# Kernel tuning notes

Hardware: AMD Instinct MI355X
Metric: run time of the kernel (lower is better)

Reference implementation:

```python
import jax, jax.numpy as jnp
import numpy as np

B, T, E, H, V = 64, 128, 256, 1024, 8000

def setup_inputs() -> dict:
    key = jax.random.key(0)
    ks = jax.random.split(key, 18)
    s = 0.1
    f = lambda k, shp: (jax.random.normal(k, shp) * s).astype(jnp.float32)
    return {
        "x": jax.random.randint(ks[0], (B, T), 0, V),
        "given_num": 64,
        "emb": f(ks[1], (V, E)),
        "Wi": f(ks[2], (E, H)), "Ui": f(ks[3], (H, H)), "bi": f(ks[4], (H,)),
        "Wf": f(ks[5], (E, H)), "Uf": f(ks[6], (H, H)), "bf": f(ks[7], (H,)),
        "Wog": f(ks[8], (E, H)), "Uog": f(ks[9], (H, H)), "bog": f(ks[10], (H,)),
        "Wc": f(ks[11], (E, H)), "Uc": f(ks[12], (H, H)), "bc": f(ks[13], (H,)),
        "Wo": f(ks[14], (H, V)), "bo": f(ks[15], (V,)),
    }

def reference(x, given_num, emb, Wi, Ui, bi, Wf, Uf, bf, Wog, Uog, bog, Wc, Uc, bc, Wo, bo):
    # NOTE: the torch source overwrites processed_x[i] AFTER it has been consumed,
    # so the recurrence is fully teacher-forced on x; sampling only fills gen_x
    # for steps >= given_num. We reproduce exactly that.
    px = jnp.transpose(emb[x], (1, 0, 2))               # [T,B,E] teacher embeddings
    Wcat = jnp.concatenate([Wi, Wf, Wog, Wc], axis=1)    # [E,4H] fused input-gate weights
    Ucat = jnp.concatenate([Ui, Uf, Uog, Uc], axis=1)    # [H,4H] fused hidden-gate weights
    bcat = jnp.concatenate([bi, bf, bog, bc])            # [4H]
    xw = jnp.einsum('tbe,eh->tbh', px, Wcat) + bcat      # [T,B,4H] one big GEMM upfront
    keys = jax.random.split(jax.random.key(1), T)        # per-step sampling keys

    def step(carry, inp):
        h, c = carry
        xw_t, i, xtok, k = inp
        z = xw_t + h @ Ucat                              # [B,4H] fused gate pre-activations
        i_g, f_g, o_g, c_hat = jnp.split(z, 4, axis=-1)
        c = jax.nn.sigmoid(f_g) * c + jax.nn.sigmoid(i_g) * jnp.tanh(c_hat)
        h = jax.nn.sigmoid(o_g) * jnp.tanh(c)
        logits = h @ Wo + bo                             # [B,V]
        samp = jax.random.categorical(k, logits)         # = multinomial over softmax
        tok = jnp.where(i < given_num, xtok, samp)
        return (h, c), tok

    h0 = jnp.zeros((B, H), jnp.float32)
    c0 = jnp.zeros((B, H), jnp.float32)
    _, toks = jax.lax.scan(step, (h0, c0), (xw, jnp.arange(T), x.T, keys))
    return toks.T                                        # [B,T] int tokens (gen_x)
```

## Files before the change

kernel.cpp:

```cpp
#include <hip/hip_runtime.h>
#include <hip/hip_cooperative_groups.h>
#include <cstdint>
#include <cstddef>

#define TT 128
#define BB 64
#define EE 256
#define HH 1024
#define VV 8000
#define LSTRIDE 132

__device__ __forceinline__ uint32_t rotl32(uint32_t v, int r){ return (v<<r)|(v>>(32-r)); }

__device__ __forceinline__ void tf2x32(uint32_t k0, uint32_t k1, uint32_t x0, uint32_t x1,
                                       uint32_t& y0, uint32_t& y1)
{
  const uint32_t k2 = k0 ^ k1 ^ 0x1BD11BDAu;
  x0 += k0; x1 += k1;
#define TFR(r) { x0 += x1; x1 = rotl32(x1,(r)); x1 ^= x0; }
  TFR(13) TFR(15) TFR(26) TFR(6)   x0 += k1; x1 += k2 + 1u;
  TFR(17) TFR(29) TFR(16) TFR(24)  x0 += k2; x1 += k0 + 2u;
  TFR(13) TFR(15) TFR(26) TFR(6)   x0 += k0; x1 += k1 + 3u;
  TFR(17) TFR(29) TFR(16) TFR(24)  x0 += k1; x1 += k2 + 4u;
  TFR(13) TFR(15) TFR(26) TFR(6)   x0 += k2; x1 += k0 + 5u;
#undef TFR
  y0 = x0; y1 = x1;
}

__device__ __forceinline__ float u01f(uint32_t bits){
  float f = __uint_as_float((bits >> 9) | 0x3f800000u) - 1.0f;
  return (f == 0.0f) ? 1.17549435e-38f : f;
}

__device__ __forceinline__ float xla_tanh(float x){
  float xc = fminf(fmaxf(x, -7.90531110763549805f), 7.90531110763549805f);
  float x2 = __fmul_rn(xc, xc);
  float num = -2.76076847742355e-16f;
  num = __fadd_rn(__fmul_rn(x2, num),  2.00018790482477e-13f);
  num = __fadd_rn(__fmul_rn(x2, num), -8.60467152213735e-11f);
  num = __fadd_rn(__fmul_rn(x2, num),  5.12229709037114e-08f);
  num = __fadd_rn(__fmul_rn(x2, num),  1.48572235717979e-05f);
  num = __fadd_rn(__fmul_rn(x2, num),  6.37261928875436e-04f);
  num = __fadd_rn(__fmul_rn(x2, num),  4.89352455891786e-03f);
  num = __fmul_rn(xc, num);
  float den = 1.19825839466702e-06f;
  den = __fadd_rn(__fmul_rn(x2, den), 1.18534705686654e-04f);
  den = __fadd_rn(__fmul_rn(x2, den), 2.26843463243900e-03f);
  den = __fadd_rn(__fmul_rn(x2, den), 4.89352518554385e-03f);
  float r = __fdiv_rn(num, den);
  return (fabsf(x) < 0.0004f) ? x : r;
}

__device__ __forceinline__ float xla_sigmoid(float x){
  float t = xla_tanh(__fmul_rn(0.5f, x));
  return __fadd_rn(0.5f, __fmul_rn(0.5f, t));
}

__device__ __forceinline__ unsigned long long pack32(float s, int v){
  uint32_t u = __float_as_uint(s);
  u = (u >> 31) ? ~u : (u | 0x80000000u);
  return ((unsigned long long)u << 32) | (unsigned)(8191 - v);
}

#define LGKM0 asm volatile("s_waitcnt lgkmcnt(0)" ::: "memory")

__global__ void initz(float* hfull, unsigned long long* best, int* flags){
  int i = blockIdx.x*256 + threadIdx.x;
  if (i < HH*BB)  hfull[i] = 0.f;
  if (i < TT*BB)  best[i] = 0ull;
  if (i < 256)    flags[i] = 0;
}

__global__ __launch_bounds__(256) void pxgen(
    const int* __restrict__ x, const float* __restrict__ emb, float* __restrict__ px)
{
  int flat = blockIdx.x*256 + threadIdx.x;
  int b = flat & 63;
  int e = (flat >> 6) & 255;
  int t = flat >> 14;
  if (t >= TT) return;
  int tok = x[b*TT + t];
  px[((size_t)t*EE + e)*BB + b] = emb[(size_t)tok*EE + e];
}

__global__ __launch_bounds__(256) void transpose4f(
    const float* __restrict__ g0, const float* __restrict__ g1,
    const float* __restrict__ g2, const float* __restrict__ g3,
    float* __restrict__ out, int R, int C)
{
  const float* in = (blockIdx.y==0)?g0:(blockIdx.y==1)?g1:(blockIdx.y==2)?g2:g3;
  int tilesC = C >> 6;
  int tr = blockIdx.x / tilesC, tc = blockIdx.x % tilesC;
  __shared__ float tile[64][65];
  int tid = threadIdx.x;
  #pragma unroll
  for (int s = 0; s < 16; ++s) {
    int li = s*256 + tid;
    int r = li >> 6, c = li & 63;
    tile[r][c] = in[(size_t)(tr*64 + r)*C + tc*64 + c];
  }
  __syncthreads();
  #pragma unroll
  for (int s = 0; s < 16; ++s) {
    int li = s*256 + tid;
    int c = li >> 6, r = li & 63;
    out[((size_t)blockIdx.y*C + tc*64 + c)*R + tr*64 + r] = tile[r][c];
  }
}

__global__ __launch_bounds__(512) void lstm_rec(
    const float* __restrict__ Wt, const float* __restrict__ Ut,
    const float* __restrict__ bi, const float* __restrict__ bf,
    const float* __restrict__ bog, const float* __restrict__ bc,
    const float* __restrict__ px, float* __restrict__ hfull,
    int* __restrict__ flags)
{
  __shared__ float sA[64*LSTRIDE];
  __shared__ float sB[64*LSTRIDE];
  __shared__ float spx[64*LSTRIDE];
  __shared__ float xch[2304];

  const int tid  = threadIdx.x;
  const int w    = tid >> 6;
  const int lane = tid & 63;
  const int p    = w & 3;
  const int kh   = w >> 2;
  const int ju   = __builtin_amdgcn_readfirstlane(blockIdx.x*4 + p);
  const int sw4  = ((lane >> 3) & 7) << 2;

  const float* Ug0 = Ut + ((size_t)0*HH + ju)*HH;
  const float* Ug1 = Ut + ((size_t)1*HH + ju)*HH;
  const float* Ug2 = Ut + ((size_t)2*HH + ju)*HH;
  const float* Ug3 = Ut + ((size_t)3*HH + ju)*HH;
  const int g0 = 2*kh, g1 = 2*kh + 1;
  const float* W0 = Wt + ((size_t)g0*HH + ju)*EE;
  const float* W1 = Wt + ((size_t)g1*HH + ju)*EE;
  const float biaA = kh ? bog[ju] : bi[ju];
  const float biaB = kh ? bc[ju]  : bf[ju];

  float c = 0.f;
  float B0 = 0.f, B1 = 0.f;
  float4 pre[4];

  auto load_chunk = [&](const float* hp, int hcn){
    #pragma unroll
    for (int s = 0; s < 4; ++s) {
      int f = s*512 + tid;
      int k = f >> 4, b0 = (f & 15)*4;
      pre[s] = *(const float4*)(hp + (size_t)(hcn*128 + k)*BB + b0);
    }
  };
  auto store_chunk = [&](float* buf){
    #pragma unroll
    for (int s = 0; s < 4; ++s) {
      int f = s*512 + tid;
      int k = f >> 4, b0 = (f & 15)*4;
      int kc = k ^ (((b0 >> 3) & 7) << 2);
      buf[(b0+0)*LSTRIDE + kc] = pre[s].x;
      buf[(b0+1)*LSTRIDE + kc] = pre[s].y;
      buf[(b0+2)*LSTRIDE + kc] = pre[s].z;
      buf[(b0+3)*LSTRIDE + kc] = pre[s].w;
    }
  };

  auto compute_xw = [&](int t2){
    float A0 = 0.f, A1 = 0.f;
    #pragma unroll 1
    for (int ch = 0; ch < 2; ++ch) {
      const float* pxc = px + ((size_t)t2*EE + ch*128)*BB;
      LGKM0;
      __builtin_amdgcn_s_barrier();
      #pragma unroll
      for (int s = 0; s < 4; ++s) {
        int f = s*512 + tid;
        int e = f >> 4, b0 = (f & 15)*4;
        float4 v = *(const float4*)(pxc + (size_t)e*BB + b0);
        int ec = e ^ (((b0 >> 3) & 7) << 2);
        spx[(b0+0)*LSTRIDE + ec] = v.x;
        spx[(b0+1)*LSTRIDE + ec] = v.y;
        spx[(b0+2)*LSTRIDE + ec] = v.z;
        spx[(b0+3)*LSTRIDE + ec] = v.w;
      }
      LGKM0;
      __builtin_amdgcn_s_barrier();
      #pragma unroll
      for (int e = 0; e < 128; e += 4) {
        float4 p4 = *(const float4*)&spx[lane*LSTRIDE + (e ^ sw4)];
        A0 = __fadd_rn(A0, __fmul_rn(p4.x, W0[ch*128 + e + 0]));
        A1 = __fadd_rn(A1, __fmul_rn(p4.x, W1[ch*128 + e + 0]));
        A0 = __fadd_rn(A0, __fmul_rn(p4.y, W0[ch*128 + e + 1]));
        A1 = __fadd_rn(A1, __fmul_rn(p4.y, W1[ch*128 + e + 1]));
        A0 = __fadd_rn(A0, __fmul_rn(p4.z, W0[ch*128 + e + 2]));
        A1 = __fadd_rn(A1, __fmul_rn(p4.z, W1[ch*128 + e + 2]));
        A0 = __fadd_rn(A0, __fmul_rn(p4.w, W0[ch*128 + e + 3]));
        A1 = __fadd_rn(A1, __fmul_rn(p4.w, W1[ch*128 + e + 3]));
      }
    }
    B0 = __fadd_rn(A0, biaA);
    B1 = __fadd_rn(A1, biaB);
  };

  compute_xw(0);

  #pragma unroll 1
  for (int t = 0; t < TT; ++t) {
    const float* hp = hfull + (size_t)t*(HH*BB);
    float*       rn = hfull + (size_t)(t+1)*(HH*BB);

    load_chunk(hp, 0);
    float R0=0.f, R1=0.f, R2=0.f, R3=0.f;
    float PA0=0.f, PA1=0.f, PA2=0.f, PA3=0.f;
    #pragma unroll 1
    for (int hc = 0; hc < 8; ++hc) {
      float* cur = (hc & 1) ? sB : sA;
      store_chunk(cur);
      if (hc < 7) load_chunk(hp, hc + 1);
      LGKM0;
      __builtin_amdgcn_s_barrier();
      int sLo = kh ? ((hc == 4) ? 2 : (hc > 4 ? 0 : 4)) : 0;
      int sHi = kh ? ((hc >= 4) ? 4 : 0)               : ((hc < 4) ? 4 : (hc == 4 ? 2 : 0));
      #pragma unroll
      for (int sub = 0; sub < 4; ++sub) {
        if (sub < sLo || sub >= sHi) continue;
        int kabs = hc*128 + sub*32;
        if (kabs == 288 || kabs == 864) {
          PA0 = R0; R0 = 0.f;
          PA1 = R1; R1 = 0.f;
          PA2 = R2; R2 = 0.f;
          PA3 = R3; R3 = 0.f;
        }
        #pragma unroll
        for (int q = sub*32; q < sub*32 + 32; q += 4) {
          float4 h4 = *(const float4*)&cur[lane*LSTRIDE + (q ^ sw4)];
          int k = hc*128 + q;
          R0 = __fadd_rn(R0, __fmul_rn(h4.x, Ug0[k+0]));
          R1 = __fadd_rn(R1, __fmul_rn(h4.x, Ug1[k+0]));
          R2 = __fadd_rn(R2, __fmul_rn(h4.x, Ug2[k+0]));
          R3 = __fadd_rn(R3, __fmul_rn(h4.x, Ug3[k+0]));
          R0 = __fadd_rn(R0, __fmul_rn(h4.y, Ug0[k+1]));
          R1 = __fadd_rn(R1, __fmul_rn(h4.y, Ug1[k+1]));
          R2 = __fadd_rn(R2, __fmul_rn(h4.y, Ug2[k+1]));
          R3 = __fadd_rn(R3, __fmul_rn(h4.y, Ug3[k+1]));
          R0 = __fadd_rn(R0, __fmul_rn(h4.z, Ug0[k+2]));
          R1 = __fadd_rn(R1, __fmul_rn(h4.z, Ug1[k+2]));
          R2 = __fadd_rn(R2, __fmul_rn(h4.z, Ug2[k+2]));
          R3 = __fadd_rn(R3, __fmul_rn(h4.z, Ug3[k+2]));
          R0 = __fadd_rn(R0, __fmul_rn(h4.w, Ug0[k+3]));
          R1 = __fadd_rn(R1, __fmul_rn(h4.w, Ug1[k+3]));
          R2 = __fadd_rn(R2, __fmul_rn(h4.w, Ug2[k+3]));
          R3 = __fadd_rn(R3, __fmul_rn(h4.w, Ug3[k+3]));
        }
      }
    }
    float keepA = 0.f, keepB = 0.f, keepC = 0.f, keepD = 0.f;
    if (kh == 0) {
      keepA = __fadd_rn(PA0, R0);
      keepB = __fadd_rn(PA1, R1);
      xch[1024 + p*64 + lane] = __fadd_rn(PA2, R2);
      xch[1280 + p*64 + lane] = __fadd_rn(PA3, R3);
    } else {
      keepA = PA2; keepB = R2;
      keepC = PA3; keepD = R3;
      xch[   0 + p*64 + lane] = PA0;
      xch[ 256 + p*64 + lane] = R0;
      xch[ 512 + p*64 + lane] = PA1;
      xch[ 768 + p*64 + lane] = R1;
    }
    LGKM0;
    __builtin_amdgcn_s_barrier();
    float z0, z1;
    if (kh == 0) {
      float T0 = __fadd_rn(__fadd_rn(keepA, xch[   0 + p*64 + lane]), xch[ 256 + p*64 + lane]);
      float T1 = __fadd_rn(__fadd_rn(keepB, xch[ 512 + p*64 + lane]), xch[ 768 + p*64 + lane]);
      z0 = __fadd_rn(B0, T0);
      z1 = __fadd_rn(B1, T1);
    } else {
      float T2 = __fadd_rn(__fadd_rn(xch[1024 + p*64 + lane], keepA), keepB);
      float T3 = __fadd_rn(__fadd_rn(xch[1280 + p*64 + lane], keepC), keepD);
      z0 = __fadd_rn(B0, T2);
      z1 = __fadd_rn(B1, T3);
    }

    float igv = 0.f, fgv = 0.f, hv = 0.f;
    if (kh) {
      float th  = xla_tanh(z1);
      float ogs = xla_sigmoid(z0);
      xch[1536 + p*64 + lane] = th;
      xch[1792 + p*64 + lane] = ogs;
    } else {
      igv = xla_sigmoid(z0);
      fgv = xla_sigmoid(z1);
    }
    LGKM0;
    __builtin_amdgcn_s_barrier();
    if (!kh) {
      float th  = xch[1536 + p*64 + lane];
      float ogs = xch[1792 + p*64 + lane];
      c = __fadd_rn(__fmul_rn(fgv, c), __fmul_rn(igv, th));
      hv = __fmul_rn(ogs, xla_tanh(c));
      __hip_atomic_store(&rn[(size_t)ju*BB + lane], hv,
                         __ATOMIC_RELAXED, __HIP_MEMORY_SCOPE_AGENT);
    }
    __syncthreads();
    if (tid == 0)
      __hip_atomic_store(&flags[blockIdx.x], t+1, __ATOMIC_RELEASE, __HIP_MEMORY_SCOPE_AGENT);

    if (t < TT-1) {
      compute_xw(t+1);
      if (w == 0) {
        for (;;) {
          int m0 = __hip_atomic_load(&flags[lane],       __ATOMIC_RELAXED, __HIP_MEMORY_SCOPE_AGENT);
          int m1 = __hip_atomic_load(&flags[64 + lane],  __ATOMIC_RELAXED, __HIP_MEMORY_SCOPE_AGENT);
          int m2 = __hip_atomic_load(&flags[128 + lane], __ATOMIC_RELAXED, __HIP_MEMORY_SCOPE_AGENT);
          int m3 = __hip_atomic_load(&flags[192 + lane], __ATOMIC_RELAXED, __HIP_MEMORY_SCOPE_AGENT);
          int mm = m0 < m1 ? m0 : m1;
          int nn = m2 < m3 ? m2 : m3;
          mm = mm < nn ? mm : nn;
          if (__all(mm >= t+1)) break;
          __builtin_amdgcn_s_sleep(1);
        }
        __atomic_signal_fence(__ATOMIC_ACQUIRE);
      }
      __syncthreads();
    }
  }
}

__global__ __launch_bounds__(256, 2) void logits_samp(
    const float* __restrict__ hfull, const float* __restrict__ Wo,
    const float* __restrict__ bo, const int* __restrict__ gnp,
    unsigned long long* __restrict__ best)
{
  const int t = 64 + blockIdx.y;
  if (t < gnp[0]) return;
  const int vt   = blockIdx.x;
  const int z    = blockIdx.z;
  const int tid  = threadIdx.x;
  const int w    = tid >> 6;
  const int lane = tid & 63;

  int v[4], vc[4]; bool val[4];
  #pragma unroll
  for (int vj = 0; vj < 4; ++vj) {
    v[vj]  = vt*1024 + vj*256 + tid;
    val[vj] = (v[vj] < VV);
    vc[vj] = val[vj] ? v[vj] : (VV-1);
  }

  __shared__ float hds[128*16];
  __shared__ unsigned long long red[4][16];

  float tot[64], reg[64];
  #pragma unroll
  for (int i = 0; i < 64; ++i) { tot[i] = 0.f; reg[i] = 0.f; }

  const float* hf = hfull + (size_t)(t+1)*(HH*BB);

  #pragma unroll 1
  for (int kc8 = 0; kc8 < 8; ++kc8) {
    __syncthreads();
    #pragma unroll
    for (int s = 0; s < 8; ++s) {
      int idx = s*256 + tid;
      int kl = idx >> 4, bb = idx & 15;
      hds[idx] = hf[(size_t)(kc8*128 + kl)*BB + z*16 + bb];
    }
    __syncthreads();
    #pragma unroll 1
    for (int sub = 0; sub < 4; ++sub) {
      int kabs = kc8*128 + sub*32;
      if (kabs == 288 || kabs == 576 || kabs == 864) {
        #pragma unroll
        for (int i = 0; i < 64; ++i) { tot[i] = __fadd_rn(tot[i], reg[i]); reg[i] = 0.f; }
      }
      #pragma unroll 2
      for (int k = sub*32; k < sub*32 + 32; ++k) {
        const float* wr = Wo + (size_t)(kc8*128 + k)*VV;
        float wv0 = wr[vc[0]], wv1 = wr[vc[1]], wv2 = wr[vc[2]], wv3 = wr[vc[3]];
        #pragma unroll
        for (int bb = 0; bb < 16; ++bb) {
          float hb = hds[k*16 + bb];
          reg[0*16+bb] = __fadd_rn(reg[0*16+bb], __fmul_rn(hb, wv0));
          reg[1*16+bb] = __fadd_rn(reg[1*16+bb], __fmul_rn(hb, wv1));
          reg[2*16+bb] = __fadd_rn(reg[2*16+bb], __fmul_rn(hb, wv2));
          reg[3*16+bb] = __fadd_rn(reg[3*16+bb], __fmul_rn(hb, wv3));
        }
      }
    }
  }
  #pragma unroll
  for (int i = 0; i < 64; ++i) tot[i] = __fadd_rn(tot[i], reg[i]);

  uint32_t kt0, kt1;
  tf2x32(0u, 1u, 0u, (uint32_t)t, kt0, kt1);
  float bov[4];
  #pragma unroll
  for (int vj = 0; vj < 4; ++vj) bov[vj] = val[vj] ? bo[v[vj]] : 0.f;

  #pragma unroll 1
  for (int bb = 0; bb < 16; ++bb) {
    int bglob = z*16 + bb;
    unsigned long long pm = 0ull;
    #pragma unroll
    for (int vj = 0; vj < 4; ++vj) {
      if (val[vj]) {
        uint32_t y0, y1;
        tf2x32(kt0, kt1, 0u, (uint32_t)(bglob*VV + v[vj]), y0, y1);
        float u  = u01f(y0 ^ y1);
        float l1 = logf(u);
        float l2 = logf(-l1);
        float g  = -l2;
        float L  = __fadd_rn(tot[vj*16 + bb], bov[vj]);
        float sc = __fadd_rn(g, L);
        unsigned long long pk = pack32(sc, v[vj]);
        if (pk > pm) pm = pk;
      }
    }
    #pragma unroll
    for (int m = 32; m > 0; m >>= 1) {
      unsigned long long q = __shfl_xor(pm, m);
      if (q > pm) pm = q;
    }
    if (lane == 0) red[w][bb] = pm;
    __syncthreads();
    if (tid == 0) {
      unsigned long long m0 = red[0][bb];
      if (red[1][bb] > m0) m0 = red[1][bb];
      if (red[2][bb] > m0) m0 = red[2][bb];
      if (red[3][bb] > m0) m0 = red[3][bb];
      atomicMax(&best[(size_t)t*BB + z*16 + bb], m0);
    }
    __syncthreads();
  }
}

__global__ void finalize(const int* __restrict__ x, const int* __restrict__ gnp,
                         const unsigned long long* __restrict__ best, int* __restrict__ out)
{
  int i = blockIdx.x*256 + threadIdx.x;
  if (i >= BB*TT) return;
  int t = i & 127;
  int b = i >> 7;
  if (t < gnp[0] || t < 64) out[i] = x[i];
  else out[i] = 8191 - (int)(best[(size_t)t*BB + b] & 0x1FFFull);
}

extern "C" void kernel_launch(void* const* d_in, const int* in_sizes, int n_in,
                              void* d_out, int out_size, void* d_ws, size_t ws_size,
                              hipStream_t stream)
{
  const int*   x    = (const int*)  d_in[0];
  const int*   gn   = (const int*)  d_in[1];
  const float* emb  = (const float*)d_in[2];
  const float* Wi   = (const float*)d_in[3];
  const float* Ui   = (const float*)d_in[4];
  const float* bi   = (const float*)d_in[5];
  const float* Wf   = (const float*)d_in[6];
  const float* Uf   = (const float*)d_in[7];
  const float* bf   = (const float*)d_in[8];
  const float* Wog  = (const float*)d_in[9];
  const float* Uog  = (const float*)d_in[10];
  const float* bog  = (const float*)d_in[11];
  const float* Wc   = (const float*)d_in[12];
  const float* Uc   = (const float*)d_in[13];
  const float* bc   = (const float*)d_in[14];
  const float* Wo   = (const float*)d_in[15];
  const float* bo   = (const float*)d_in[16];

  float* Ut    = (float*)d_ws;
  float* Wt    = Ut + (size_t)4*1024*1024;
  float* hfull = Wt + (size_t)1024*1024;
  float* px    = hfull + (size_t)(TT+1)*HH*BB;
  unsigned long long* best =
      (unsigned long long*)(px + (size_t)TT*EE*BB);
  int* flags  = (int*)(best + (size_t)TT*BB);

  initz<<<512, 256, 0, stream>>>(hfull, best, flags);
  transpose4f<<<dim3(256,4), 256, 0, stream>>>(Ui, Uf, Uog, Uc, Ut, 1024, 1024);
  transpose4f<<<dim3(64,4),  256, 0, stream>>>(Wi, Wf, Wog, Wc, Wt, 256, 1024);
  pxgen<<<8192, 256, 0, stream>>>(x, emb, px);

  const float* Wtp = Wt; const float* Utp = Ut;
  const float* bip = bi; const float* bfp = bf; const float* bogp = bog; const float* bcp = bc;
  const float* pxp = px; float* hfullp = hfull; int* flagsp = flags;
  void* kargs[] = { (void*)&Wtp, (void*)&Utp,
                    (void*)&bip, (void*)&bfp, (void*)&bogp, (void*)&bcp,
                    (void*)&pxp, (void*)&hfullp, (void*)&flagsp };
  hipLaunchCooperativeKernel((void*)lstm_rec, dim3(256), dim3(512), kargs, 0, stream);

  logits_samp<<<dim3(8,64,4), 256, 0, stream>>>(hfull, Wo, bo, gn, best);
  finalize<<<32, 256, 0, stream>>>(x, gn, best, (int*)d_out);
}
```

Measured before the change: 6.239 ms.

## Pre-tile embeddings so xw projection reads float4s directly, dropping LDS staging

The embedding gather kernel now writes px in a tiled layout [t][b/16][e/4][b%16][4], so each lane can load its batch row's float4 of embedding values straight from global memory. The input projection inside the recurrent kernel drops the shared-memory staging buffer and its two barriers per chunk, which removes LDS traffic and block syncs from every timestep. In exchange, each wave issues more global loads per step and relies on cache hits, and LDS use shrinks, which may change occupancy or scheduling.

```diff
diff --git a/kernel.cpp b/kernel.cpp
--- a/kernel.cpp
+++ b/kernel.cpp
@@ -72,15 +72,16 @@
 }
 
 __global__ __launch_bounds__(256) void pxgen(
-    const int* __restrict__ x, const float* __restrict__ emb, float* __restrict__ px)
+    const int* __restrict__ x, const float* __restrict__ emb, float* __restrict__ pxT)
 {
   int flat = blockIdx.x*256 + threadIdx.x;
-  int b = flat & 63;
-  int e = (flat >> 6) & 255;
+  int e = flat & 255;
+  int b = (flat >> 8) & 63;
   int t = flat >> 14;
   if (t >= TT) return;
   int tok = x[b*TT + t];
-  px[((size_t)t*EE + e)*BB + b] = emb[(size_t)tok*EE + e];
+  size_t fi = ((((size_t)t*4 + (b>>4))*64 + (e>>2))*16 + (size_t)(b&15))*4 + (e&3);
+  pxT[fi] = emb[(size_t)tok*EE + e];
 }
 
 __global__ __launch_bounds__(256) void transpose4f(
@@ -112,12 +113,11 @@
     const float* __restrict__ Wt, const float* __restrict__ Ut,
     const float* __restrict__ bi, const float* __restrict__ bf,
     const float* __restrict__ bog, const float* __restrict__ bc,
-    const float* __restrict__ px, float* __restrict__ hfull,
+    const float* __restrict__ pxT, float* __restrict__ hfull,
     int* __restrict__ flags)
 {
   __shared__ float sA[64*LSTRIDE];
   __shared__ float sB[64*LSTRIDE];
-  __shared__ float spx[64*LSTRIDE];
   __shared__ float xch[2304];
 
   const int tid  = threadIdx.x;
@@ -127,6 +127,7 @@
   const int kh   = w >> 2;
   const int ju   = __builtin_amdgcn_readfirstlane(blockIdx.x*4 + p);
   const int sw4  = ((lane >> 3) & 7) << 2;
+  const int lgrp = lane >> 4, l16 = lane & 15;
 
   const float* Ug0 = Ut + ((size_t)0*HH + ju)*HH;
   const float* Ug1 = Ut + ((size_t)1*HH + ju)*HH;
@@ -165,35 +166,22 @@
 
   auto compute_xw = [&](int t2){
     float A0 = 0.f, A1 = 0.f;
+    const float4* pb = (const float4*)pxT + (((size_t)t2*4 + lgrp)*64)*16 + l16;
     #pragma unroll 1
-    for (int ch = 0; ch < 2; ++ch) {
-      const float* pxc = px + ((size_t)t2*EE + ch*128)*BB;
-      LGKM0;
-      __builtin_amdgcn_s_barrier();
+    for (int ec = 0; ec < 8; ++ec) {
       #pragma unroll
-      for (int s = 0; s < 4; ++s) {
-        int f = s*512 + tid;
-        int e = f >> 4, b0 = (f & 15)*4;
-        float4 v = *(const float4*)(pxc + (size_t)e*BB + b0);
-        int ec = e ^ (((b0 >> 3) & 7) << 2);
-        spx[(b0+0)*LSTRIDE + ec] = v.x;
-        spx[(b0+1)*LSTRIDE + ec] = v.y;
-        spx[(b0+2)*LSTRIDE + ec] = v.z;
-        spx[(b0+3)*LSTRIDE + ec] = v.w;
-      }
-      LGKM0;
-      __builtin_amdgcn_s_barrier();
-      #pragma unroll
-      for (int e = 0; e < 128; e += 4) {
-        float4 p4 = *(const float4*)&spx[lane*LSTRIDE + (e ^ sw4)];
-        A0 = __fadd_rn(A0, __fmul_rn(p4.x, W0[ch*128 + e + 0]));
-        A1 = __fadd_rn(A1, __fmul_rn(p4.x, W1[ch*128 + e + 0]));
-        A0 = __fadd_rn(A0, __fmul_rn(p4.y, W0[ch*128 + e + 1]));
-        A1 = __fadd_rn(A1, __fmul_rn(p4.y, W1[ch*128 + e + 1]));
-        A0 = __fadd_rn(A0, __fmul_rn(p4.z, W0[ch*128 + e + 2]));
-        A1 = __fadd_rn(A1, __fmul_rn(p4.z, W1[ch*128 + e + 2]));
-        A0 = __fadd_rn(A0, __fmul_rn(p4.w, W0[ch*128 + e + 3]));
-        A1 = __fadd_rn(A1, __fmul_rn(p4.w, W1[ch*128 + e + 3]));
+      for (int j = 0; j < 8; ++j) {
+        int eq = ec*8 + j;
+        float4 v = pb[(size_t)eq*16];
+        int e = eq*4;
+        A0 = __fadd_rn(A0, __fmul_rn(v.x, W0[e+0]));
+        A1 = __fadd_rn(A1, __fmul_rn(v.x, W1[e+0]));
+        A0 = __fadd_rn(A0, __fmul_rn(v.y, W0[e+1]));
+        A1 = __fadd_rn(A1, __fmul_rn(v.y, W1[e+1]));
+        A0 = __fadd_rn(A0, __fmul_rn(v.z, W0[e+2]));
+        A1 = __fadd_rn(A1, __fmul_rn(v.z, W1[e+2]));
+        A0 = __fadd_rn(A0, __fmul_rn(v.w, W0[e+3]));
+        A1 = __fadd_rn(A1, __fmul_rn(v.w, W1[e+3]));
       }
     }
     B0 = __fadd_rn(A0, biaA);
@@ -470,19 +458,19 @@
   float* Ut    = (float*)d_ws;
   float* Wt    = Ut + (size_t)4*1024*1024;
   float* hfull = Wt + (size_t)1024*1024;
-  float* px    = hfull + (size_t)(TT+1)*HH*BB;
+  float* pxT   = hfull + (size_t)(TT+1)*HH*BB;
   unsigned long long* best =
-      (unsigned long long*)(px + (size_t)TT*EE*BB);
+      (unsigned long long*)(pxT + (size_t)TT*EE*BB);
   int* flags  = (int*)(best + (size_t)TT*BB);
 
   initz<<<512, 256, 0, stream>>>(hfull, best, flags);
   transpose4f<<<dim3(256,4), 256, 0, stream>>>(Ui, Uf, Uog, Uc, Ut, 1024, 1024);
   transpose4f<<<dim3(64,4),  256, 0, stream>>>(Wi, Wf, Wog, Wc, Wt, 256, 1024);
-  pxgen<<<8192, 256, 0, stream>>>(x, emb, px);
+  pxgen<<<8192, 256, 0, stream>>>(x, emb, pxT);
 
   const float* Wtp = Wt; const float* Utp = Ut;
   const float* bip = bi; const float* bfp = bf; const float* bogp = bog; const float* bcp = bc;
-  const float* pxp = px; float* hfullp = hfull; int* flagsp = flags;
+  const float* pxp = pxT; float* hfullp = hfull; int* flagsp = flags;
   void* kargs[] = { (void*)&Wtp, (void*)&Utp,
                     (void*)&bip, (void*)&bfp, (void*)&bogp, (void*)&bcp,
                     (void*)&pxp, (void*)&hfullp, (void*)&flagsp };
```

Result: slower. 6.495 ms (+4.1%).
